# Kernel optimization log

Measured on AMD Instinct MI355X. Metric: run time of the kernel, lower is better.

Reference implementation:

```python
import jax, jax.numpy as jnp
import numpy as np

B, T, N_X, N_U, N_Y, H = 2048, 2048, 4, 2, 1, 64
MIN_X = jnp.array([0.0, 0.0, 0.0, -jnp.inf], dtype=jnp.float32)
MAX_X = jnp.array([10.0, 10.0, 10.0, jnp.inf], dtype=jnp.float32)
MIN_Y = jnp.array([0.0], dtype=jnp.float32)
MAX_Y = jnp.array([10.0], dtype=jnp.float32)


def setup_inputs() -> dict:
    key = jax.random.key(0)
    ks = jax.random.split(key, 6)
    return {
        "x_0": jax.random.uniform(ks[0], (B, N_X), dtype=jnp.float32) * 5.0,
        "u": jax.random.normal(ks[1], (B, T, N_U), dtype=jnp.float32),
        "theta_f": jnp.array([0.1925, 0.2429, 0.1697, 0.0444, 0.1642], dtype=jnp.float32),
        "theta_h": jnp.zeros((1,), dtype=jnp.float32),
        "tau_u": jnp.ones((1,), dtype=jnp.float32),
        "tau_y": jnp.ones((1,), dtype=jnp.float32),
        "W1": jax.random.normal(ks[2], (N_X + N_U + 5, H), dtype=jnp.float32) / np.sqrt(N_X + N_U + 5),
        "b1": jnp.zeros((H,), dtype=jnp.float32),
        "W2": jax.random.normal(ks[3], (H, N_X), dtype=jnp.float32) * 0.05,
        "Wh": jax.random.normal(ks[4], (N_X, N_Y), dtype=jnp.float32),
    }


def reference(x_0, u, theta_f, theta_h, tau_u, tau_y, W1, b1, W2, Wh):
    Bc = x_0.shape[0]
    tf = jnp.broadcast_to(theta_f[None, :], (Bc, theta_f.shape[0]))
    scale = tau_u[0] / tau_y[0]

    def f(x, ut):
        feat = jnp.concatenate([x, ut, tf], axis=-1)  # (B, n_x+n_u+5)
        return jnp.tanh(feat @ W1 + b1) @ W2 * scale  # (B, n_x)

    def h(x):
        return x @ Wh + theta_h  # (B, n_y)

    y0 = h(x_0)  # unclamped initial output, as in the torch loop

    def step(carry, ut):
        x_step, y_step = carry
        dx = f(x_step, ut)
        x_raw = x_step + dx
        y_new = jnp.clip(h(x_raw), MIN_Y, MAX_Y)  # y computed from pre-clamp state
        x_new = jnp.clip(x_raw, MIN_X, MAX_X)
        return (x_new, y_new), (x_step, y_step)

    u_t = jnp.moveaxis(u, 1, 0)  # (T, B, n_u)
    _, (xs, ys) = jax.lax.scan(step, (x_0, y0), u_t)
    x = jnp.moveaxis(xs, 0, 1)  # (B, T, n_x)
    y = jnp.moveaxis(ys, 0, 1)  # (B, T, n_y)
    return (x, y)
```

## Files before the change

kernel.cpp:

```cpp
#include <hip/hip_runtime.h>

#define B_SZ 2048
#define T_SZ 2048

using f32x16 = float __attribute__((ext_vector_type(16)));

template<int CTRL>
__device__ __forceinline__ float dppf(float v) {
  int r = __builtin_amdgcn_update_dpp(0, __builtin_bit_cast(int, v), CTRL, 0xf, 0xf, true);
  return __builtin_bit_cast(float, r);
}

__device__ __forceinline__ float swz16(float v) {
  return __builtin_bit_cast(float,
      __builtin_amdgcn_ds_swizzle(__builtin_bit_cast(int, v), 0x401F));
}

__device__ __forceinline__ float bperm(int addr_bytes, float v) {
  return __builtin_bit_cast(float,
      __builtin_amdgcn_ds_bpermute(addr_bytes, __builtin_bit_cast(int, v)));
}

__global__ __launch_bounds__(256, 2) void sss_kernel(
    const float* __restrict__ x0p, const float* __restrict__ up,
    const float* __restrict__ tfp, const float* __restrict__ thp,
    const float* __restrict__ tup, const float* __restrict__ typ,
    const float* __restrict__ W1p, const float* __restrict__ b1p,
    const float* __restrict__ W2p, const float* __restrict__ Whp,
    float* __restrict__ outp)
{
  const int lane = threadIdx.x & 63;
  const int wv   = __builtin_amdgcn_readfirstlane((int)(threadIdx.x >> 6));
  const int b    = blockIdx.x * 4 + wv;

  const float w1x0 = W1p[0 * 64 + lane];
  const float w1x1 = W1p[1 * 64 + lane];
  const float w1x2 = W1p[2 * 64 + lane];
  const float w1x3 = W1p[3 * 64 + lane];
  const float w1u0 = W1p[4 * 64 + lane];
  const float w1u1 = W1p[5 * 64 + lane];

  float cc = b1p[lane];
#pragma unroll
  for (int j = 0; j < 5; ++j)
    cc = fmaf(tfp[j], W1p[(6 + j) * 64 + lane], cc);

  const float scale = tup[0] / typ[0];
  const float4 w2r = ((const float4*)W2p)[lane];
  const float w2_0 = w2r.x * scale;
  const float w2_1 = w2r.y * scale;
  const float w2_2 = w2r.z * scale;
  const float w2_3 = w2r.w * scale;
  const bool lb0 = lane & 1;
  const bool lb1 = (lane >> 1) & 1;
  const float w2A = lb0 ? w2_1 : w2_0;
  const float w2B = lb0 ? w2_0 : w2_1;
  const float w2C = lb0 ? w2_3 : w2_2;
  const float w2D = lb0 ? w2_2 : w2_3;

  const float wh0 = Whp[0], wh1 = Whp[1], wh2 = Whp[2], wh3 = Whp[3];
  const float th  = thp[0];

  float x0v = x0p[b * 4 + 0];
  float x1v = x0p[b * 4 + 1];
  float x2v = x0p[b * 4 + 2];
  float x3v = x0p[b * 4 + 3];
  float yv = fmaf(x3v, wh3, fmaf(x2v, wh2, fmaf(x1v, wh1, fmaf(x0v, wh0, th))));

  const f32x16* up16 = (const f32x16*)(up + (size_t)b * (T_SZ * 2));
  float* outx = outp + (size_t)b * (T_SZ * 4);
  float* outy = outp + (size_t)B_SZ * T_SZ * 4 + (size_t)b * T_SZ;

  const int addr32 = (lane ^ 32) << 2;
  const int addr48 = (lane ^ 48) << 2;

  f32x16 uch = up16[0];
  const int gmax = T_SZ / 8 - 1;

  for (int blk = 0; blk < T_SZ; blk += 64) {
    float bx0 = 0.f, bx1 = 0.f, bx2 = 0.f, bx3 = 0.f, byv = 0.f;
#pragma unroll 2
    for (int seg = 0; seg < 8; ++seg) {
      int g = (blk >> 3) + seg + 1;
      g = g > gmax ? gmax : g;
      const f32x16 unx = up16[g];
      const int wbase = seg * 8;
#pragma unroll
      for (int j = 0; j < 8; ++j) {
        const bool m = (lane == wbase + j);
        bx0 = m ? x0v : bx0;
        bx1 = m ? x1v : bx1;
        bx2 = m ? x2v : bx2;
        bx3 = m ? x3v : bx3;
        byv = m ? yv  : byv;

        const float u0 = uch[2 * j];
        const float u1 = uch[2 * j + 1];

        float acc = fmaf(u0, w1u0, cc);
        acc = fmaf(u1, w1u1, acc);
        acc = fmaf(x0v, w1x0, acc);
        acc = fmaf(x1v, w1x1, acc);
        acc = fmaf(x2v, w1x2, acc);
        acc = fmaf(x3v, w1x3, acc);

        const float e  = __builtin_amdgcn_exp2f(acc * 2.8853900817779268f);
        const float rr = __builtin_amdgcn_rcpf(e + 1.0f);
        const float h  = fmaf(-2.0f, rr, 1.0f);

        const float pA = h * w2A, pB = h * w2B, pC = h * w2C, pD = h * w2D;
        const float r0 = pA + dppf<0xB1>(pB);
        const float r1 = pC + dppf<0xB1>(pD);
        const float keep = lb1 ? r1 : r0;
        const float send = lb1 ? r0 : r1;
        float v = keep + dppf<0x4E>(send);
        v += dppf<0x124>(v);
        v += dppf<0x128>(v);
        const float a16 = swz16(v);
        const float a32 = bperm(addr32, v);
        const float a48 = bperm(addr48, v);
        v = (v + a16) + (a32 + a48);

        const float dx0 = dppf<0x00>(v);
        const float dx1 = dppf<0x55>(v);
        const float dx2 = dppf<0xAA>(v);
        const float dx3 = dppf<0xFF>(v);

        const float xr0 = x0v + dx0;
        const float xr1 = x1v + dx1;
        const float xr2 = x2v + dx2;
        const float xr3 = x3v + dx3;

        float t0 = fmaf(xr1, wh1, fmaf(xr0, wh0, th));
        float t1 = fmaf(xr3, wh3, xr2 * wh2);
        yv = __builtin_amdgcn_fmed3f(t0 + t1, 0.0f, 10.0f);

        x0v = __builtin_amdgcn_fmed3f(xr0, 0.0f, 10.0f);
        x1v = __builtin_amdgcn_fmed3f(xr1, 0.0f, 10.0f);
        x2v = __builtin_amdgcn_fmed3f(xr2, 0.0f, 10.0f);
        x3v = xr3;
      }
      uch = unx;
    }
    float4 bx;
    bx.x = bx0; bx.y = bx1; bx.z = bx2; bx.w = bx3;
    *(float4*)(outx + (size_t)(blk + lane) * 4) = bx;
    outy[blk + lane] = byv;
  }
}

extern "C" void kernel_launch(void* const* d_in, const int* in_sizes, int n_in,
                              void* d_out, int out_size, void* d_ws, size_t ws_size,
                              hipStream_t stream) {
  (void)in_sizes; (void)n_in; (void)out_size; (void)d_ws; (void)ws_size;
  sss_kernel<<<dim3(B_SZ / 4), dim3(256), 0, stream>>>(
      (const float*)d_in[0], (const float*)d_in[1], (const float*)d_in[2],
      (const float*)d_in[3], (const float*)d_in[4], (const float*)d_in[5],
      (const float*)d_in[6], (const float*)d_in[7], (const float*)d_in[8],
      (const float*)d_in[9], (float*)d_out);
}
```

Before: 416.5 us.

## Fold tanh constant into weights, lane-distribute state, and store per step

```diff
diff --git a/kernel.cpp b/kernel.cpp
--- a/kernel.cpp
+++ b/kernel.cpp
@@ -33,17 +33,19 @@
   const int wv   = __builtin_amdgcn_readfirstlane((int)(threadIdx.x >> 6));
   const int b    = blockIdx.x * 4 + wv;
 
-  const float w1x0 = W1p[0 * 64 + lane];
-  const float w1x1 = W1p[1 * 64 + lane];
-  const float w1x2 = W1p[2 * 64 + lane];
-  const float w1x3 = W1p[3 * 64 + lane];
-  const float w1u0 = W1p[4 * 64 + lane];
-  const float w1u1 = W1p[5 * 64 + lane];
+  const float K = 2.8853900817779268f;
+  const float w1x0 = W1p[0 * 64 + lane] * K;
+  const float w1x1 = W1p[1 * 64 + lane] * K;
+  const float w1x2 = W1p[2 * 64 + lane] * K;
+  const float w1x3 = W1p[3 * 64 + lane] * K;
+  const float w1u0 = W1p[4 * 64 + lane] * K;
+  const float w1u1 = W1p[5 * 64 + lane] * K;
 
   float cc = b1p[lane];
 #pragma unroll
   for (int j = 0; j < 5; ++j)
     cc = fmaf(tfp[j], W1p[(6 + j) * 64 + lane], cc);
+  cc *= K;
 
   const float scale = tup[0] / typ[0];
   const float4 w2r = ((const float4*)W2p)[lane];
@@ -58,94 +60,94 @@
   const float w2C = lb0 ? w2_3 : w2_2;
   const float w2D = lb0 ? w2_2 : w2_3;
 
-  const float wh0 = Whp[0], wh1 = Whp[1], wh2 = Whp[2], wh3 = Whp[3];
+  const float whl = Whp[lane & 3];
   const float th  = thp[0];
 
-  float x0v = x0p[b * 4 + 0];
-  float x1v = x0p[b * 4 + 1];
-  float x2v = x0p[b * 4 + 2];
-  float x3v = x0p[b * 4 + 3];
-  float yv = fmaf(x3v, wh3, fmaf(x2v, wh2, fmaf(x1v, wh1, fmaf(x0v, wh0, th))));
+  const float lo = ((lane & 3) == 3) ? -__builtin_inff() : 0.0f;
+  const float hi = ((lane & 3) == 3) ?  __builtin_inff() : 10.0f;
 
-  const f32x16* up16 = (const f32x16*)(up + (size_t)b * (T_SZ * 2));
-  float* outx = outp + (size_t)b * (T_SZ * 4);
-  float* outy = outp + (size_t)B_SZ * T_SZ * 4 + (size_t)b * T_SZ;
+  float xlane = x0p[b * 4 + (lane & 3)];
+  float x0v = dppf<0x00>(xlane);
+  float x1v = dppf<0x55>(xlane);
+  float x2v = dppf<0xAA>(xlane);
+  float x3v = dppf<0xFF>(xlane);
+
+  float p0 = xlane * whl;
+  p0 += dppf<0xB1>(p0);
+  p0 += dppf<0x4E>(p0);
+  float yv = p0 + th;
+
+  unsigned voff, vinc;
+  if (lane < 4) {
+    voff = (unsigned)(b * (T_SZ * 4) + lane) * 4u;
+    vinc = 16u;
+  } else {
+    voff = (unsigned)((unsigned)B_SZ * T_SZ * 4u + (unsigned)b * T_SZ) * 4u;
+    vinc = (lane == 4) ? 4u : 0u;
+  }
+  const bool doSt = (lane < 5);
+  const bool is4  = (lane == 4);
 
   const int addr32 = (lane ^ 32) << 2;
   const int addr48 = (lane ^ 48) << 2;
 
+  const f32x16* up16 = (const f32x16*)(up + (size_t)b * (T_SZ * 2));
+  char* outB = (char*)outp;
+
   f32x16 uch = up16[0];
-  const int gmax = T_SZ / 8 - 1;
+  const int NC = T_SZ / 8;
 
-  for (int blk = 0; blk < T_SZ; blk += 64) {
-    float bx0 = 0.f, bx1 = 0.f, bx2 = 0.f, bx3 = 0.f, byv = 0.f;
-#pragma unroll 2
-    for (int seg = 0; seg < 8; ++seg) {
-      int g = (blk >> 3) + seg + 1;
-      g = g > gmax ? gmax : g;
-      const f32x16 unx = up16[g];
-      const int wbase = seg * 8;
+  for (int c = 0; c < NC; ++c) {
+    const int g = (c + 1 < NC) ? c + 1 : NC - 1;
+    const f32x16 unx = up16[g];
 #pragma unroll
-      for (int j = 0; j < 8; ++j) {
-        const bool m = (lane == wbase + j);
-        bx0 = m ? x0v : bx0;
-        bx1 = m ? x1v : bx1;
-        bx2 = m ? x2v : bx2;
-        bx3 = m ? x3v : bx3;
-        byv = m ? yv  : byv;
+    for (int j = 0; j < 8; ++j) {
+      const float vdata = is4 ? yv : xlane;
+      if (doSt) *(float*)(outB + voff) = vdata;
+      voff += vinc;
 
-        const float u0 = uch[2 * j];
-        const float u1 = uch[2 * j + 1];
+      const float u0 = uch[2 * j];
+      const float u1 = uch[2 * j + 1];
 
-        float acc = fmaf(u0, w1u0, cc);
-        acc = fmaf(u1, w1u1, acc);
-        acc = fmaf(x0v, w1x0, acc);
-        acc = fmaf(x1v, w1x1, acc);
-        acc = fmaf(x2v, w1x2, acc);
-        acc = fmaf(x3v, w1x3, acc);
+      float a0 = fmaf(u0, w1u0, cc);
+      a0 = fmaf(x0v, w1x0, a0);
+      a0 = fmaf(x2v, w1x2, a0);
+      float a1 = u1 * w1u1;
+      a1 = fmaf(x1v, w1x1, a1);
+      a1 = fmaf(x3v, w1x3, a1);
+      const float acc = a0 + a1;
 
-        const float e  = __builtin_amdgcn_exp2f(acc * 2.8853900817779268f);
-        const float rr = __builtin_amdgcn_rcpf(e + 1.0f);
-        const float h  = fmaf(-2.0f, rr, 1.0f);
+      const float e  = __builtin_amdgcn_exp2f(acc);
+      const float rr = __builtin_amdgcn_rcpf(e + 1.0f);
+      const float h  = fmaf(-2.0f, rr, 1.0f);
 
-        const float pA = h * w2A, pB = h * w2B, pC = h * w2C, pD = h * w2D;
-        const float r0 = pA + dppf<0xB1>(pB);
-        const float r1 = pC + dppf<0xB1>(pD);
-        const float keep = lb1 ? r1 : r0;
-        const float send = lb1 ? r0 : r1;
-        float v = keep + dppf<0x4E>(send);
-        v += dppf<0x124>(v);
-        v += dppf<0x128>(v);
-        const float a16 = swz16(v);
-        const float a32 = bperm(addr32, v);
-        const float a48 = bperm(addr48, v);
-        v = (v + a16) + (a32 + a48);
+      const float pA = h * w2A, pB = h * w2B, pC = h * w2C, pD = h * w2D;
+      const float r0 = pA + dppf<0xB1>(pB);
+      const float r1 = pC + dppf<0xB1>(pD);
+      const float keep = lb1 ? r1 : r0;
+      const float send = lb1 ? r0 : r1;
+      float v = keep + dppf<0x4E>(send);
+      v += dppf<0x124>(v);
+      v += dppf<0x128>(v);
+      const float a16 = swz16(v);
+      const float a32 = bperm(addr32, v);
+      const float a48 = bperm(addr48, v);
+      v = (v + a16) + (a32 + a48);
 
-        const float dx0 = dppf<0x00>(v);
-        const float dx1 = dppf<0x55>(v);
-        const float dx2 = dppf<0xAA>(v);
-        const float dx3 = dppf<0xFF>(v);
+      const float w = xlane + v;
+      xlane = __builtin_amdgcn_fmed3f(w, lo, hi);
 
-        const float xr0 = x0v + dx0;
-        const float xr1 = x1v + dx1;
-        const float xr2 = x2v + dx2;
-        const float xr3 = x3v + dx3;
+      float p = w * whl;
+      p += dppf<0xB1>(p);
+      p += dppf<0x4E>(p);
+      yv = __builtin_amdgcn_fmed3f(p + th, 0.0f, 10.0f);
 
-        float t0 = fmaf(xr1, wh1, fmaf(xr0, wh0, th));
-        float t1 = fmaf(xr3, wh3, xr2 * wh2);
-        yv = __builtin_amdgcn_fmed3f(t0 + t1, 0.0f, 10.0f);
-
-        x0v = __builtin_amdgcn_fmed3f(xr0, 0.0f, 10.0f);
-        x1v = __builtin_amdgcn_fmed3f(xr1, 0.0f, 10.0f);
-        x2v = __builtin_amdgcn_fmed3f(xr2, 0.0f, 10.0f);
-        x3v = xr3;
-      }
-      uch = unx;
+      x0v = dppf<0x00>(xlane);
+      x1v = dppf<0x55>(xlane);
+      x2v = dppf<0xAA>(xlane);
+      x3v = dppf<0xFF>(xlane);
     }
-    float4 bx;
-    bx.x = bx0; bx.y = bx1; bx.z = bx2; bx.w = bx3;
-    *(float4*)(outx + (size_t)(blk + lane) * 4) = bx;
-    outy[blk + lane] = byv;
+    uch = unx;
   }
 }
 
```

Result: faster. 389.5 us (-6.5%).
